# Optimization experiments

Hardware: AMD Instinct MI355X
Metric: run time of the kernel (lower is better)

The kernel has to match this reference:

```python
import jax, jax.numpy as jnp
import numpy as np

NUM_HEADS = 16
LN_EPS = 1e-5


def _layer_norm(x, g, b):
    m = x.mean(-1, keepdims=True)
    v = x.var(-1, keepdims=True)
    return (x - m) / jnp.sqrt(v + LN_EPS) * g + b


def setup_inputs() -> dict:
    key = jax.random.key(0)
    ks = jax.random.split(key, 4)
    Bq, Bk, Nk, C = 128, 128, 256, 1024
    return {
        "qx": jax.random.normal(ks[0], (Bq, 1, C), jnp.float32),
        "kx": jax.random.normal(ks[1], (Bk, Nk, C), jnp.float32),
        "gq": jnp.ones((C,), jnp.float32),
        "bq": jnp.zeros((C,), jnp.float32),
        "gk": jnp.ones((C,), jnp.float32),
        "bk": jnp.zeros((C,), jnp.float32),
        "Wq": jax.random.normal(ks[2], (C, C), jnp.float32) * (C ** -0.5),
        "Wk": jax.random.normal(ks[3], (C, C), jnp.float32) * (C ** -0.5),
    }


def reference(qx, kx, gq, bq, gk, bk, Wq, Wk):
    H = NUM_HEADS
    Bq, _, C = qx.shape  # qx: [Bq, 1, C]
    Bk, Nk, _ = kx.shape  # kx: [Bk, Nk, C]
    hd = C // H
    scale = hd ** -0.5
    # LayerNorm + linear projections (nn.Linear: x @ W.T, no bias)
    q = (_layer_norm(qx, gq, bq) @ Wq.T).reshape(Bq, H, hd)       # [Bq, H, hd] (Nq=1 squeezed)
    k = (_layer_norm(kx, gk, bk) @ Wk.T).reshape(Bk, Nk, H, hd)   # [Bk, Nk, H, hd]
    # Full bipartite cross-batch attention scores: [Bq, Bk, H, Nk]
    attn = jnp.einsum('qhc,knhc->qkhn', q, k) * scale
    attn = jax.nn.softmax(attn, axis=-1)
    # v = kx broadcast over heads in original einsum 'khnc,qkhn->qkc';
    # equivalent: sum attn over heads, then contract over Nk.
    w = attn.sum(axis=2)                                           # [Bq, Bk, Nk]
    x = jnp.einsum('knc,qkn->qkc', kx, w)                          # [Bq, Bk, C]
    return x
```

## Files before the change

kernel.cpp:

```cpp
#include <hip/hip_runtime.h>


typedef unsigned short ushort_t;
typedef __bf16 bf16x8 __attribute__((ext_vector_type(8)));
typedef float f32x4 __attribute__((ext_vector_type(4)));

#define AS1 __attribute__((address_space(1)))
#define AS3 __attribute__((address_space(3)))

__device__ __forceinline__ void gload_lds16(const void* g, void* l) {
  __builtin_amdgcn_global_load_lds((const AS1 unsigned int*)g, (AS3 unsigned int*)l, 16, 0, 0);
}

__device__ __forceinline__ ushort_t f2bf(float f) {
  unsigned u = __float_as_uint(f);
  unsigned r = u + 0x7FFFu + ((u >> 16) & 1u);
  return (ushort_t)(r >> 16);
}

__global__ __launch_bounds__(256) void cvt_bf16_kernel(const float* __restrict__ src,
                                                       ushort_t* __restrict__ dst, int n4) {
  int i = blockIdx.x * 256 + threadIdx.x;
  if (i < n4) {
    float4 v = ((const float4*)src)[i];
    ushort4 o;
    o.x = f2bf(v.x); o.y = f2bf(v.y); o.z = f2bf(v.z); o.w = f2bf(v.w);
    ((ushort4*)dst)[i] = o;
  }
}

__global__ __launch_bounds__(256) void ln_kernel(const float* __restrict__ kx,
                                                 const float* __restrict__ qx,
                                                 const float* __restrict__ gk,
                                                 const float* __restrict__ bk,
                                                 const float* __restrict__ gq,
                                                 const float* __restrict__ bq,
                                                 const float* __restrict__ WqF,
                                                 ushort_t* __restrict__ kln,
                                                 ushort_t* __restrict__ qproj) {
  const int tid = threadIdx.x, lane = tid & 63, wid = tid >> 6;

  if (blockIdx.x < 128) {
    const int ti = blockIdx.x * 4 + wid;
    const int mq = ti >> 6, nq = ti & 63;
    const int g = lane >> 4, rr = lane & 15;

    float s = 0.f, s2 = 0.f;
    {
      const float* p = qx + (size_t)(mq * 16 + (lane & 15)) * 1024 + (lane >> 4) * 256;
      #pragma unroll 8
      for (int i = 0; i < 64; ++i) {
        float4 v = ((const float4*)p)[i];
        s  += v.x + v.y + v.z + v.w;
        s2 += v.x*v.x + v.y*v.y + v.z*v.z + v.w*v.w;
      }
    }
    s  += __shfl_xor(s, 16);  s2 += __shfl_xor(s2, 16);
    s  += __shfl_xor(s, 32);  s2 += __shfl_xor(s2, 32);
    const float mean = s * (1.0f / 1024.0f);
    const float var  = s2 * (1.0f / 1024.0f) - mean * mean;
    const float rstd = rsqrtf(var + 1e-5f);

    const float* qa = qx  + (size_t)(mq * 16 + rr) * 1024;
    const float* wb = WqF + (size_t)(nq * 16 + rr) * 1024;

    f32x4 qacc0 = (f32x4){0.f, 0.f, 0.f, 0.f};
    f32x4 qacc1 = (f32x4){0.f, 0.f, 0.f, 0.f};
    #pragma unroll 4
    for (int kk = 0; kk < 32; kk += 2) {
      #pragma unroll
      for (int e = 0; e < 2; ++e) {
        const int co = (kk + e) * 32 + g * 8;
        float4 a0 = *(const float4*)(qa + co);
        float4 a1 = *(const float4*)(qa + co + 4);
        float4 g0 = *(const float4*)(gq + co);
        float4 g1 = *(const float4*)(gq + co + 4);
        float4 b0 = *(const float4*)(bq + co);
        float4 b1 = *(const float4*)(bq + co + 4);
        float4 w0 = *(const float4*)(wb + co);
        float4 w1 = *(const float4*)(wb + co + 4);
        bf16x8 af, bf;
        af[0] = (__bf16)((a0.x - mean) * rstd * g0.x + b0.x);
        af[1] = (__bf16)((a0.y - mean) * rstd * g0.y + b0.y);
        af[2] = (__bf16)((a0.z - mean) * rstd * g0.z + b0.z);
        af[3] = (__bf16)((a0.w - mean) * rstd * g0.w + b0.w);
        af[4] = (__bf16)((a1.x - mean) * rstd * g1.x + b1.x);
        af[5] = (__bf16)((a1.y - mean) * rstd * g1.y + b1.y);
        af[6] = (__bf16)((a1.z - mean) * rstd * g1.z + b1.z);
        af[7] = (__bf16)((a1.w - mean) * rstd * g1.w + b1.w);
        bf[0] = (__bf16)w0.x; bf[1] = (__bf16)w0.y; bf[2] = (__bf16)w0.z; bf[3] = (__bf16)w0.w;
        bf[4] = (__bf16)w1.x; bf[5] = (__bf16)w1.y; bf[6] = (__bf16)w1.z; bf[7] = (__bf16)w1.w;
        if (e == 0) qacc0 = __builtin_amdgcn_mfma_f32_16x16x32_bf16(af, bf, qacc0, 0, 0, 0);
        else        qacc1 = __builtin_amdgcn_mfma_f32_16x16x32_bf16(af, bf, qacc1, 0, 0, 0);
      }
    }
    #pragma unroll
    for (int rg = 0; rg < 4; ++rg)
      qproj[(size_t)(mq * 16 + (g << 2) + rg) * 1024 + nq * 16 + rr] =
          f2bf(qacc0[rg] + qacc1[rg]);
    return;
  }

  const int row = (blockIdx.x - 128) * 4 + wid;
  const float* src = kx + (size_t)row * 1024;
  ushort_t* dst = kln + (size_t)row * 1024;
  const int c0 = lane * 4;

  float4 v0 = *(const float4*)(src + c0);
  float4 v1 = *(const float4*)(src + c0 + 256);
  float4 v2 = *(const float4*)(src + c0 + 512);
  float4 v3 = *(const float4*)(src + c0 + 768);

  float s  = (v0.x + v0.y + v0.z + v0.w) + (v1.x + v1.y + v1.z + v1.w)
           + (v2.x + v2.y + v2.z + v2.w) + (v3.x + v3.y + v3.z + v3.w);
  float s2 = (v0.x*v0.x + v0.y*v0.y + v0.z*v0.z + v0.w*v0.w)
           + (v1.x*v1.x + v1.y*v1.y + v1.z*v1.z + v1.w*v1.w)
           + (v2.x*v2.x + v2.y*v2.y + v2.z*v2.z + v2.w*v2.w)
           + (v3.x*v3.x + v3.y*v3.y + v3.z*v3.z + v3.w*v3.w);
  #pragma unroll
  for (int off = 1; off < 64; off <<= 1) {
    s  += __shfl_xor(s, off);
    s2 += __shfl_xor(s2, off);
  }
  const float mean = s * (1.0f / 1024.0f);
  const float var  = s2 * (1.0f / 1024.0f) - mean * mean;
  const float rstd = rsqrtf(var + 1e-5f);

  float4 g0 = *(const float4*)(gk + c0);
  float4 g1 = *(const float4*)(gk + c0 + 256);
  float4 g2 = *(const float4*)(gk + c0 + 512);
  float4 g3 = *(const float4*)(gk + c0 + 768);
  float4 b0 = *(const float4*)(bk + c0);
  float4 b1 = *(const float4*)(bk + c0 + 256);
  float4 b2 = *(const float4*)(bk + c0 + 512);
  float4 b3 = *(const float4*)(bk + c0 + 768);

  ushort4 o0, o1, o2, o3;
  o0.x = f2bf((v0.x - mean) * rstd * g0.x + b0.x);
  o0.y = f2bf((v0.y - mean) * rstd * g0.y + b0.y);
  o0.z = f2bf((v0.z - mean) * rstd * g0.z + b0.z);
  o0.w = f2bf((v0.w - mean) * rstd * g0.w + b0.w);
  o1.x = f2bf((v1.x - mean) * rstd * g1.x + b1.x);
  o1.y = f2bf((v1.y - mean) * rstd * g1.y + b1.y);
  o1.z = f2bf((v1.z - mean) * rstd * g1.z + b1.z);
  o1.w = f2bf((v1.w - mean) * rstd * g1.w + b1.w);
  o2.x = f2bf((v2.x - mean) * rstd * g2.x + b2.x);
  o2.y = f2bf((v2.y - mean) * rstd * g2.y + b2.y);
  o2.z = f2bf((v2.z - mean) * rstd * g2.z + b2.z);
  o2.w = f2bf((v2.w - mean) * rstd * g2.w + b2.w);
  o3.x = f2bf((v3.x - mean) * rstd * g3.x + b3.x);
  o3.y = f2bf((v3.y - mean) * rstd * g3.y + b3.y);
  o3.z = f2bf((v3.z - mean) * rstd * g3.z + b3.z);
  o3.w = f2bf((v3.w - mean) * rstd * g3.w + b3.w);

  *(ushort4*)(dst + c0)       = o0;
  *(ushort4*)(dst + c0 + 256) = o1;
  *(ushort4*)(dst + c0 + 512) = o2;
  *(ushort4*)(dst + c0 + 768) = o3;
}

__global__ __launch_bounds__(512, 2) void gemm256_kernel(const ushort_t* __restrict__ A,
                                                         const ushort_t* __restrict__ Bt,
                                                         ushort_t* __restrict__ Cpk,
                                                         int M, int N) {
  __shared__ ushort_t lds[4][2][256 * 32];

  const int tid = threadIdx.x, lane = tid & 63, wid = tid >> 6;
  const int g = lane >> 4, rr = lane & 15;
  const int wr = wid >> 2, wc = wid & 3;

  const int Mt = M >> 8, Nt = N >> 8;
  const int nwg = Mt * Nt;
  const int qq = nwg >> 3, r8 = nwg & 7;
  const int xcd = blockIdx.x & 7, idx = blockIdx.x >> 3;
  const int wg = (xcd < r8 ? xcd * (qq + 1) : r8 * (qq + 1) + (xcd - r8) * qq) + idx;
  const int mt = wg / Nt, nt = wg - mt * Nt;
  const size_t m0 = (size_t)mt << 8, n0 = (size_t)nt << 8;

  const int s_r  = lane >> 2;
  const int s_gr = (lane & 3) ^ (s_r & 3);

  const ushort_t* Abase = A  + m0 * 1024;
  const ushort_t* Bbase = Bt + n0 * 1024;

  f32x4 acc[8][4];
  #pragma unroll
  for (int i = 0; i < 8; ++i)
    #pragma unroll
    for (int j = 0; j < 4; ++j) acc[i][j] = (f32x4){0.f, 0.f, 0.f, 0.f};

  auto stageA = [&](int kt) {
    const int k0 = kt << 5;
    ushort_t* dst = &lds[kt & 3][0][0];
    #pragma unroll
    for (int it = 0; it < 2; ++it) {
      int ci = (wid << 1) | it;
      int r  = (ci << 4) + s_r;
      gload_lds16(Abase + (size_t)r * 1024 + k0 + (s_gr << 3), dst + (ci << 9));
    }
  };
  auto stageB = [&](int kt) {
    const int k0 = kt << 5;
    ushort_t* dst = &lds[kt & 3][1][0];
    #pragma unroll
    for (int it = 0; it < 2; ++it) {
      int ci = (wid << 1) | it;
      int r  = (ci << 4) + s_r;
      gload_lds16(Bbase + (size_t)r * 1024 + k0 + (s_gr << 3), dst + (ci << 9));
    }
  };

  stageA(0); stageB(0); stageA(1); stageB(1); stageA(2); stageB(2);
  asm volatile("s_waitcnt vmcnt(8)" ::: "memory");
  __builtin_amdgcn_s_barrier();

  const int rsw = rr & 3;

  #pragma unroll 1
  for (int u = 0; u < 29; ++u) {
    const ushort_t* as = &lds[u & 3][0][0];
    const ushort_t* bs = &lds[u & 3][1][0];
    bf16x8 af[8];
    {
      #pragma unroll
      for (int i = 0; i < 8; ++i) {
        int r = (wr << 7) + (i << 4) + rr;
        af[i] = *(const bf16x8*)&as[(r << 5) + ((g ^ rsw) << 3)];
      }
      int r0 = (wc << 6) + rr;
      bf16x8 b0 = *(const bf16x8*)&bs[(r0 << 5) + ((g ^ rsw) << 3)];
      int r1 = (wc << 6) + 16 + rr;
      bf16x8 b1 = *(const bf16x8*)&bs[(r1 << 5) + ((g ^ rsw) << 3)];
      stageA(u + 3);
      __builtin_amdgcn_s_setprio(1);
      #pragma unroll
      for (int i = 0; i < 8; ++i) {
        acc[i][0] = __builtin_amdgcn_mfma_f32_16x16x32_bf16(af[i], b0, acc[i][0], 0, 0, 0);
        acc[i][1] = __builtin_amdgcn_mfma_f32_16x16x32_bf16(af[i], b1, acc[i][1], 0, 0, 0);
      }
      __builtin_amdgcn_s_setprio(0);
      __builtin_amdgcn_s_barrier();
    }
    {
      int r2 = (wc << 6) + 32 + rr;
      bf16x8 b2 = *(const bf16x8*)&bs[(r2 << 5) + ((g ^ rsw) << 3)];
      int r3 = (wc << 6) + 48 + rr;
      bf16x8 b3 = *(const bf16x8*)&bs[(r3 << 5) + ((g ^ rsw) << 3)];
      stageB(u + 3);
      __builtin_amdgcn_s_setprio(1);
      #pragma unroll
      for (int i = 0; i < 8; ++i) {
        acc[i][2] = __builtin_amdgcn_mfma_f32_16x16x32_bf16(af[i], b2, acc[i][2], 0, 0, 0);
        acc[i][3] = __builtin_amdgcn_mfma_f32_16x16x32_bf16(af[i], b3, acc[i][3], 0, 0, 0);
      }
      __builtin_amdgcn_s_setprio(0);
      asm volatile("s_waitcnt vmcnt(8)" ::: "memory");
      __builtin_amdgcn_s_barrier();
    }
  }

  asm volatile("s_waitcnt vmcnt(0)" ::: "memory");
  __builtin_amdgcn_s_barrier();
  #pragma unroll 1
  for (int u = 29; u < 32; ++u) {
    const ushort_t* as = &lds[u & 3][0][0];
    const ushort_t* bs = &lds[u & 3][1][0];
    bf16x8 af2[8], bfj[4];
    #pragma unroll
    for (int i = 0; i < 8; ++i) {
      int r = (wr << 7) + (i << 4) + rr;
      af2[i] = *(const bf16x8*)&as[(r << 5) + ((g ^ rsw) << 3)];
    }
    #pragma unroll
    for (int j = 0; j < 4; ++j) {
      int r = (wc << 6) + (j << 4) + rr;
      bfj[j] = *(const bf16x8*)&bs[(r << 5) + ((g ^ rsw) << 3)];
    }
    #pragma unroll
    for (int i = 0; i < 8; ++i)
      #pragma unroll
      for (int j = 0; j < 4; ++j)
        acc[i][j] = __builtin_amdgcn_mfma_f32_16x16x32_bf16(af2[i], bfj[j], acc[i][j], 0, 0, 0);
  }

  #pragma unroll
  for (int i = 0; i < 8; ++i)
    #pragma unroll
    for (int j = 0; j < 4; ++j)
      #pragma unroll
      for (int rg = 0; rg < 4; ++rg) {
        size_t row = m0 + (wr << 7) + (i << 4) + (g << 2) + rg;
        size_t col = n0 + (wc << 6) + (j << 4) + rr;
        int kb = (int)(row >> 8), t = (int)((row >> 4) & 15), r16 = (int)(row & 15);
        int h = (int)(col >> 6), ch = (int)(col & 63);
        size_t odx = ((((size_t)kb * 16 + h) * 16 + t) << 10)
                   + ((ch >> 5) << 9) + (((ch >> 3) & 3) << 7) + (r16 << 3) + (ch & 7);
        Cpk[odx] = f2bf(acc[i][j][rg]);
      }
}

__global__ __launch_bounds__(256, 3) void scores_kernel(const ushort_t* __restrict__ qp,
                                                        const ushort_t* __restrict__ kpk,
                                                        ushort_t* __restrict__ wbuf) {
  __shared__ float pbuf[2][16][258];

  const int tid = threadIdx.x, lane = tid & 63, wid = tid >> 6;
  const int g = lane >> 4, rr = lane & 15;

  const int b = blockIdx.x;
  const int wg = (b & 7) * 128 + (b >> 3);
  const int kb = wg >> 3;
  const int q0 = (wg & 7) << 4;

  const int hs = wid;

  float w_acc[16][4];
  #pragma unroll
  for (int t = 0; t < 16; ++t)
    #pragma unroll
    for (int r = 0; r < 4; ++r) w_acc[t][r] = 0.f;

  const ushort_t* qrow = qp + (size_t)(q0 + rr) * 1024;
  const ushort_t* kbb  = kpk + ((size_t)kb * 16) * 16384 + g * 128 + rr * 8;

  for (int hp = 0; hp < 4; ++hp) {
    const int h = hp * 4 + hs;
    const int co = h * 64 + g * 8;
    bf16x8 aq0 = *(const bf16x8*)(qrow + co);
    bf16x8 aq1 = *(const bf16x8*)(qrow + co + 32);
    const ushort_t* hb = kbb + (size_t)h * 16384;
    f32x4 s[16];
    #pragma unroll
    for (int t = 0; t < 16; ++t) {
      bf16x8 b0 = *(const bf16x8*)(hb + t * 1024);
      bf16x8 b1 = *(const bf16x8*)(hb + t * 1024 + 512);
      f32x4 a = (f32x4){0.f, 0.f, 0.f, 0.f};
      a = __builtin_amdgcn_mfma_f32_16x16x32_bf16(aq0, b0, a, 0, 0, 0);
      a = __builtin_amdgcn_mfma_f32_16x16x32_bf16(aq1, b1, a, 0, 0, 0);
      s[t] = a;
    }
    #pragma unroll
    for (int r = 0; r < 4; ++r) {
      float mx = s[0][r];
      #pragma unroll
      for (int t = 1; t < 16; ++t) mx = fmaxf(mx, s[t][r]);
      mx = fmaxf(mx, __shfl_xor(mx, 1));
      mx = fmaxf(mx, __shfl_xor(mx, 2));
      mx = fmaxf(mx, __shfl_xor(mx, 4));
      mx = fmaxf(mx, __shfl_xor(mx, 8));
      float sum = 0.f;
      float e[16];
      #pragma unroll
      for (int t = 0; t < 16; ++t) {
        e[t] = __expf((s[t][r] - mx) * 0.125f);
        sum += e[t];
      }
      sum += __shfl_xor(sum, 1);
      sum += __shfl_xor(sum, 2);
      sum += __shfl_xor(sum, 4);
      sum += __shfl_xor(sum, 8);
      float inv = 1.0f / sum;
      #pragma unroll
      for (int t = 0; t < 16; ++t) w_acc[t][r] += e[t] * inv;
    }
  }

  __syncthreads();
  if (hs >= 2) {
    #pragma unroll
    for (int t = 0; t < 16; ++t)
      #pragma unroll
      for (int r = 0; r < 4; ++r)
        pbuf[hs - 2][(g << 2) + r][t * 16 + rr] = w_acc[t][r];
  }
  __syncthreads();
  if (hs < 2) {
    #pragma unroll
    for (int t = 0; t < 16; ++t)
      #pragma unroll
      for (int r = 0; r < 4; ++r)
        w_acc[t][r] += pbuf[hs][(g << 2) + r][t * 16 + rr];
    if (hs == 1) {
      #pragma unroll
      for (int t = 0; t < 16; ++t)
        #pragma unroll
        for (int r = 0; r < 4; ++r)
          pbuf[1][(g << 2) + r][t * 16 + rr] = w_acc[t][r];
    }
  }
  __syncthreads();
  if (hs == 0) {
    ushort_t* wb = wbuf + (size_t)kb * 32768;
    #pragma unroll
    for (int t = 0; t < 16; ++t)
      #pragma unroll
      for (int r = 0; r < 4; ++r) {
        float v = w_acc[t][r] + pbuf[1][(g << 2) + r][t * 16 + rr];
        wb[(size_t)(q0 + (g << 2) + r) * 256 + t * 16 + rr] = f2bf(v);
      }
  }
}

__global__ __launch_bounds__(256, 4) void pv_kernel(const ushort_t* __restrict__ wbuf,
                                                    const float* __restrict__ kx,
                                                    float* __restrict__ xout) {
  const int tid = threadIdx.x, lane = tid & 63, wid = tid >> 6;
  const int g = lane >> 4, rr = lane & 15;

  const int b = blockIdx.x;
  const int wg = (b & 7) * 128 + (b >> 3);
  const int kb = wg >> 3;
  const int c0 = (wg & 7) * 128;

  const int wr = wid >> 1, wc = wid & 1;

  f32x4 acc[4][4];
  #pragma unroll
  for (int i = 0; i < 4; ++i)
    #pragma unroll
    for (int j = 0; j < 4; ++j) acc[i][j] = (f32x4){0.f, 0.f, 0.f, 0.f};

  const ushort_t* wb = wbuf + (size_t)kb * 32768;
  const float* kxb = kx + (size_t)kb * 256 * 1024;

  for (int nc = 0; nc < 8; ++nc) {
    const int n0 = nc * 32 + g * 8;
    bf16x8 af[4];
    #pragma unroll
    for (int i = 0; i < 4; ++i) {
      int q = (wr << 6) + (i << 4) + rr;
      af[i] = *(const bf16x8*)(wb + (size_t)q * 256 + n0);
    }
    #pragma unroll
    for (int j = 0; j < 4; ++j) {
      int c = c0 + (wc << 6) + (j << 4) + rr;
      const float* src = kxb + (size_t)n0 * 1024 + c;
      float f[8];
      #pragma unroll
      for (int jj = 0; jj < 8; ++jj) f[jj] = src[(size_t)jj * 1024];
      bf16x8 bb;
      #pragma unroll
      for (int jj = 0; jj < 8; ++jj) bb[jj] = (__bf16)f[jj];
      #pragma unroll
      for (int i = 0; i < 4; ++i)
        acc[i][j] = __builtin_amdgcn_mfma_f32_16x16x32_bf16(af[i], bb, acc[i][j], 0, 0, 0);
    }
  }

  #pragma unroll
  for (int i = 0; i < 4; ++i)
    #pragma unroll
    for (int j = 0; j < 4; ++j)
      #pragma unroll
      for (int rg = 0; rg < 4; ++rg) {
        int q = (wr << 6) + (i << 4) + (g << 2) + rg;
        int c = c0 + (wc << 6) + (j << 4) + rr;
        xout[((size_t)q * 128 + kb) * 1024 + c] = acc[i][j][rg];
      }
}

extern "C" void kernel_launch(void* const* d_in, const int* in_sizes, int n_in,
                              void* d_out, int out_size, void* d_ws, size_t ws_size,
                              hipStream_t stream) {
  const float* qx = (const float*)d_in[0];
  const float* kx = (const float*)d_in[1];
  const float* gq = (const float*)d_in[2];
  const float* bq = (const float*)d_in[3];
  const float* gk = (const float*)d_in[4];
  const float* bk = (const float*)d_in[5];
  const float* Wq = (const float*)d_in[6];
  const float* Wk = (const float*)d_in[7];

  char* ws = (char*)d_ws;
  ushort_t* kkp   = (ushort_t*)(ws);
  ushort_t* qproj = (ushort_t*)(ws + 67108864);
  ushort_t* wbuf  = (ushort_t*)(ws + 67371008);
  ushort_t* Wkb   = (ushort_t*)(ws + 67371008 + 2359296);
  ushort_t* kln  = (ushort_t*)d_out;
  float*    xout = (float*)d_out;

  cvt_bf16_kernel<<<1024, 256, 0, stream>>>(Wk, Wkb, 262144);
  ln_kernel<<<128 + 8192, 256, 0, stream>>>(kx, qx, gk, bk, gq, bq, Wq, kln, qproj);
  gemm256_kernel<<<512, 512, 0, stream>>>(kln, Wkb, kkp, 32768, 1024);
  scores_kernel<<<1024, 256, 0, stream>>>(qproj, kkp, wbuf);
  pv_kernel<<<1024, 256, 0, stream>>>(wbuf, kx, xout);
}
```

Measured before the change: 268.8 us.

## Stage kx tiles through swizzled LDS in pv_kernel and fuse Wk conversion into LN launch

The PV kernel previously read kx from global memory with strided scalar loads, eight rows apart per lane. It now loads 32x128 fp32 tiles with coalesced float4 loads into double-buffered, XOR-swizzled LDS, prefetching the next tile into registers, and builds the MFMA B fragments from LDS. Separately, the Wk fp32-to-bf16 conversion becomes extra blocks of the LN kernel, which removes one launch. The cost is 32KB of LDS per block plus a barrier each iteration, which may lower occupancy under launch_bounds(256,4).

```diff
diff --git a/kernel.cpp b/kernel.cpp
--- a/kernel.cpp
+++ b/kernel.cpp
@@ -16,17 +16,6 @@
   unsigned u = __float_as_uint(f);
   unsigned r = u + 0x7FFFu + ((u >> 16) & 1u);
   return (ushort_t)(r >> 16);
-}
-
-__global__ __launch_bounds__(256) void cvt_bf16_kernel(const float* __restrict__ src,
-                                                       ushort_t* __restrict__ dst, int n4) {
-  int i = blockIdx.x * 256 + threadIdx.x;
-  if (i < n4) {
-    float4 v = ((const float4*)src)[i];
-    ushort4 o;
-    o.x = f2bf(v.x); o.y = f2bf(v.y); o.z = f2bf(v.z); o.w = f2bf(v.w);
-    ((ushort4*)dst)[i] = o;
-  }
 }
 
 __global__ __launch_bounds__(256) void ln_kernel(const float* __restrict__ kx,
@@ -36,9 +25,20 @@
                                                  const float* __restrict__ gq,
                                                  const float* __restrict__ bq,
                                                  const float* __restrict__ WqF,
+                                                 const float* __restrict__ WkF,
+                                                 ushort_t* __restrict__ Wkb,
                                                  ushort_t* __restrict__ kln,
                                                  ushort_t* __restrict__ qproj) {
   const int tid = threadIdx.x, lane = tid & 63, wid = tid >> 6;
+
+  if (blockIdx.x >= 8320) {
+    int i = (blockIdx.x - 8320) * 256 + tid;
+    float4 v = ((const float4*)WkF)[i];
+    ushort4 o;
+    o.x = f2bf(v.x); o.y = f2bf(v.y); o.z = f2bf(v.z); o.w = f2bf(v.w);
+    ((ushort4*)Wkb)[i] = o;
+    return;
+  }
 
   if (blockIdx.x < 128) {
     const int ti = blockIdx.x * 4 + wid;
@@ -404,6 +404,8 @@
 __global__ __launch_bounds__(256, 4) void pv_kernel(const ushort_t* __restrict__ wbuf,
                                                     const float* __restrict__ kx,
                                                     float* __restrict__ xout) {
+  __shared__ float kxs[2][32][128];
+
   const int tid = threadIdx.x, lane = tid & 63, wid = tid >> 6;
   const int g = lane >> 4, rr = lane & 15;
 
@@ -414,6 +416,10 @@
 
   const int wr = wid >> 1, wc = wid & 1;
 
+  const int srow = tid >> 3;
+  const int sgran = tid & 7;
+  const int swz = (srow >> 3) << 2;
+
   f32x4 acc[4][4];
   #pragma unroll
   for (int i = 0; i < 4; ++i)
@@ -421,9 +427,32 @@
     for (int j = 0; j < 4; ++j) acc[i][j] = (f32x4){0.f, 0.f, 0.f, 0.f};
 
   const ushort_t* wb = wbuf + (size_t)kb * 32768;
-  const float* kxb = kx + (size_t)kb * 256 * 1024;
-
+  const float* kxb = kx + ((size_t)kb * 256) * 1024 + c0;
+
+  float4 stg[4];
+  {
+    const float* srcrow = kxb + (size_t)srow * 1024;
+    #pragma unroll
+    for (int l = 0; l < 4; ++l) stg[l] = *(const float4*)(srcrow + ((sgran + l * 8) << 2));
+  }
+
+  #pragma unroll 1
   for (int nc = 0; nc < 8; ++nc) {
+    {
+      float* dstrow = &kxs[nc & 1][srow][0];
+      #pragma unroll
+      for (int l = 0; l < 4; ++l) {
+        int cgp = (sgran + l * 8) ^ swz;
+        *(float4*)(dstrow + (cgp << 2)) = stg[l];
+      }
+    }
+    if (nc < 7) {
+      const float* srcrow = kxb + (size_t)((nc + 1) * 32 + srow) * 1024;
+      #pragma unroll
+      for (int l = 0; l < 4; ++l) stg[l] = *(const float4*)(srcrow + ((sgran + l * 8) << 2));
+    }
+    __syncthreads();
+
     const int n0 = nc * 32 + g * 8;
     bf16x8 af[4];
     #pragma unroll
@@ -431,16 +460,14 @@
       int q = (wr << 6) + (i << 4) + rr;
       af[i] = *(const bf16x8*)(wb + (size_t)q * 256 + n0);
     }
+    const float (*kt)[128] = kxs[nc & 1];
     #pragma unroll
     for (int j = 0; j < 4; ++j) {
-      int c = c0 + (wc << 6) + (j << 4) + rr;
-      const float* src = kxb + (size_t)n0 * 1024 + c;
-      float f[8];
-      #pragma unroll
-      for (int jj = 0; jj < 8; ++jj) f[jj] = src[(size_t)jj * 1024];
+      int cl = (wc << 6) + (j << 4) + rr;
+      int cidx = ((((cl >> 2) ^ (g << 2)) << 2) + (cl & 3));
       bf16x8 bb;
       #pragma unroll
-      for (int jj = 0; jj < 8; ++jj) bb[jj] = (__bf16)f[jj];
+      for (int jj = 0; jj < 8; ++jj) bb[jj] = (__bf16)kt[(g << 3) + jj][cidx];
       #pragma unroll
       for (int i = 0; i < 4; ++i)
         acc[i][j] = __builtin_amdgcn_mfma_f32_16x16x32_bf16(af[i], bb, acc[i][j], 0, 0, 0);
@@ -479,8 +506,8 @@
   ushort_t* kln  = (ushort_t*)d_out;
   float*    xout = (float*)d_out;
 
-  cvt_bf16_kernel<<<1024, 256, 0, stream>>>(Wk, Wkb, 262144);
-  ln_kernel<<<128 + 8192, 256, 0, stream>>>(kx, qx, gk, bk, gq, bq, Wq, kln, qproj);
+  ln_kernel<<<128 + 8192 + 1024, 256, 0, stream>>>(kx, qx, gk, bk, gq, bq, Wq, Wk,
+                                                   Wkb, kln, qproj);
   gemm256_kernel<<<512, 512, 0, stream>>>(kln, Wkb, kkp, 32768, 1024);
   scores_kernel<<<1024, 256, 0, stream>>>(qproj, kkp, wbuf);
   pv_kernel<<<1024, 256, 0, stream>>>(wbuf, kx, xout);
```

Measured after the change: 275.1 us. +2.4%, slower.

## Double K-tile depth in projection GEMM with asymmetric A/B LDS buffering

Applied to the files above, without the earlier changes.

Reworks the bf16 GEMM main loop to stage 64-wide K slices instead of 32-wide ones. A is triple-buffered and B double-buffered in LDS, with a new XOR swizzle. Each K step now uses one wait plus barrier instead of two barriers, and a separate tail loop is no longer needed. This is meant to cut synchronization overhead and raise the number of MFMAs issued per barrier. In exchange, LDS use rises to 160KB and prefetch runs only one to two stages ahead, which may expose global-load latency.

```diff
diff --git a/kernel.cpp b/kernel.cpp
--- a/kernel.cpp
+++ b/kernel.cpp
@@ -163,7 +163,8 @@
                                                          const ushort_t* __restrict__ Bt,
                                                          ushort_t* __restrict__ Cpk,
                                                          int M, int N) {
-  __shared__ ushort_t lds[4][2][256 * 32];
+  __shared__ ushort_t Abuf[3][16384];
+  __shared__ ushort_t Bbuf[2][16384];
 
   const int tid = threadIdx.x, lane = tid & 63, wid = tid >> 6;
   const int g = lane >> 4, rr = lane & 15;
@@ -177,9 +178,6 @@
   const int mt = wg / Nt, nt = wg - mt * Nt;
   const size_t m0 = (size_t)mt << 8, n0 = (size_t)nt << 8;
 
-  const int s_r  = lane >> 2;
-  const int s_gr = (lane & 3) ^ (s_r & 3);
-
   const ushort_t* Abase = A  + m0 * 1024;
   const ushort_t* Bbase = Bt + n0 * 1024;
 
@@ -189,98 +187,87 @@
     #pragma unroll
     for (int j = 0; j < 4; ++j) acc[i][j] = (f32x4){0.f, 0.f, 0.f, 0.f};
 
-  auto stageA = [&](int kt) {
-    const int k0 = kt << 5;
-    ushort_t* dst = &lds[kt & 3][0][0];
-    #pragma unroll
-    for (int it = 0; it < 2; ++it) {
-      int ci = (wid << 1) | it;
-      int r  = (ci << 4) + s_r;
-      gload_lds16(Abase + (size_t)r * 1024 + k0 + (s_gr << 3), dst + (ci << 9));
+  auto stA = [&](int kt) {
+    ushort_t* dst = &Abuf[kt % 3][0];
+    #pragma unroll
+    for (int l = 0; l < 4; ++l) {
+      int ix = l * 512 + tid;
+      int r  = ix >> 3;
+      int gs = (ix & 7) ^ (((r >> 2) & 1) << 1);
+      gload_lds16(Abase + (size_t)r * 1024 + (kt << 6) + (gs << 3), dst + ix * 8);
     }
   };
-  auto stageB = [&](int kt) {
-    const int k0 = kt << 5;
-    ushort_t* dst = &lds[kt & 3][1][0];
-    #pragma unroll
-    for (int it = 0; it < 2; ++it) {
-      int ci = (wid << 1) | it;
-      int r  = (ci << 4) + s_r;
-      gload_lds16(Bbase + (size_t)r * 1024 + k0 + (s_gr << 3), dst + (ci << 9));
+  auto stB = [&](int kt) {
+    ushort_t* dst = &Bbuf[kt & 1][0];
+    #pragma unroll
+    for (int l = 0; l < 4; ++l) {
+      int ix = l * 512 + tid;
+      int r  = ix >> 3;
+      int gs = (ix & 7) ^ (((r >> 2) & 1) << 1);
+      gload_lds16(Bbase + (size_t)r * 1024 + (kt << 6) + (gs << 3), dst + ix * 8);
     }
   };
 
-  stageA(0); stageB(0); stageA(1); stageB(1); stageA(2); stageB(2);
-  asm volatile("s_waitcnt vmcnt(8)" ::: "memory");
+  stA(0); stB(0); stA(1);
+  asm volatile("s_waitcnt vmcnt(4)" ::: "memory");
   __builtin_amdgcn_s_barrier();
 
-  const int rsw = rr & 3;
+  const int sw = ((rr >> 2) & 1) << 1;
 
   #pragma unroll 1
-  for (int u = 0; u < 29; ++u) {
-    const ushort_t* as = &lds[u & 3][0][0];
-    const ushort_t* bs = &lds[u & 3][1][0];
-    bf16x8 af[8];
+  for (int j = 0; j < 16; ++j) {
+    const ushort_t* as = &Abuf[j % 3][0];
+    const ushort_t* bs = &Bbuf[j & 1][0];
+
     {
+      bf16x8 af[8], bf[4];
       #pragma unroll
       for (int i = 0; i < 8; ++i) {
         int r = (wr << 7) + (i << 4) + rr;
-        af[i] = *(const bf16x8*)&as[(r << 5) + ((g ^ rsw) << 3)];
-      }
-      int r0 = (wc << 6) + rr;
-      bf16x8 b0 = *(const bf16x8*)&bs[(r0 << 5) + ((g ^ rsw) << 3)];
-      int r1 = (wc << 6) + 16 + rr;
-      bf16x8 b1 = *(const bf16x8*)&bs[(r1 << 5) + ((g ^ rsw) << 3)];
-      stageA(u + 3);
+        af[i] = *(const bf16x8*)&as[(r << 6) + ((g ^ sw) << 3)];
+      }
+      #pragma unroll
+      for (int jj = 0; jj < 4; ++jj) {
+        int r = (wc << 6) + (jj << 4) + rr;
+        bf[jj] = *(const bf16x8*)&bs[(r << 6) + ((g ^ sw) << 3)];
+      }
+      if (j < 15) stB(j + 1);
+      if (j < 14) stA(j + 2);
       __builtin_amdgcn_s_setprio(1);
       #pragma unroll
+      for (int i = 0; i < 8; ++i)
+        #pragma unroll
+        for (int jj = 0; jj < 4; ++jj)
+          acc[i][jj] = __builtin_amdgcn_mfma_f32_16x16x32_bf16(af[i], bf[jj], acc[i][jj], 0, 0, 0);
+      __builtin_amdgcn_s_setprio(0);
+    }
+    {
+      bf16x8 af[8], bf[4];
+      #pragma unroll
       for (int i = 0; i < 8; ++i) {
-        acc[i][0] = __builtin_amdgcn_mfma_f32_16x16x32_bf16(af[i], b0, acc[i][0], 0, 0, 0);
-        acc[i][1] = __builtin_amdgcn_mfma_f32_16x16x32_bf16(af[i], b1, acc[i][1], 0, 0, 0);
-      }
+        int r = (wr << 7) + (i << 4) + rr;
+        af[i] = *(const bf16x8*)&as[(r << 6) + (((4 + g) ^ sw) << 3)];
+      }
+      #pragma unroll
+      for (int jj = 0; jj < 4; ++jj) {
+        int r = (wc << 6) + (jj << 4) + rr;
+        bf[jj] = *(const bf16x8*)&bs[(r << 6) + (((4 + g) ^ sw) << 3)];
+      }
+      __builtin_amdgcn_s_setprio(1);
+      #pragma unroll
+      for (int i = 0; i < 8; ++i)
+        #pragma unroll
+        for (int jj = 0; jj < 4; ++jj)
+          acc[i][jj] = __builtin_amdgcn_mfma_f32_16x16x32_bf16(af[i], bf[jj], acc[i][jj], 0, 0, 0);
       __builtin_amdgcn_s_setprio(0);
-      __builtin_amdgcn_s_barrier();
-    }
-    {
-      int r2 = (wc << 6) + 32 + rr;
-      bf16x8 b2 = *(const bf16x8*)&bs[(r2 << 5) + ((g ^ rsw) << 3)];
-      int r3 = (wc << 6) + 48 + rr;
-      bf16x8 b3 = *(const bf16x8*)&bs[(r3 << 5) + ((g ^ rsw) << 3)];
-      stageB(u + 3);
-      __builtin_amdgcn_s_setprio(1);
-      #pragma unroll
-      for (int i = 0; i < 8; ++i) {
-        acc[i][2] = __builtin_amdgcn_mfma_f32_16x16x32_bf16(af[i], b2, acc[i][2], 0, 0, 0);
-        acc[i][3] = __builtin_amdgcn_mfma_f32_16x16x32_bf16(af[i], b3, acc[i][3], 0, 0, 0);
-      }
-      __builtin_amdgcn_s_setprio(0);
-      asm volatile("s_waitcnt vmcnt(8)" ::: "memory");
-      __builtin_amdgcn_s_barrier();
-    }
-  }
-
-  asm volatile("s_waitcnt vmcnt(0)" ::: "memory");
-  __builtin_amdgcn_s_barrier();
-  #pragma unroll 1
-  for (int u = 29; u < 32; ++u) {
-    const ushort_t* as = &lds[u & 3][0][0];
-    const ushort_t* bs = &lds[u & 3][1][0];
-    bf16x8 af2[8], bfj[4];
-    #pragma unroll
-    for (int i = 0; i < 8; ++i) {
-      int r = (wr << 7) + (i << 4) + rr;
-      af2[i] = *(const bf16x8*)&as[(r << 5) + ((g ^ rsw) << 3)];
-    }
-    #pragma unroll
-    for (int j = 0; j < 4; ++j) {
-      int r = (wc << 6) + (j << 4) + rr;
-      bfj[j] = *(const bf16x8*)&bs[(r << 5) + ((g ^ rsw) << 3)];
-    }
-    #pragma unroll
-    for (int i = 0; i < 8; ++i)
-      #pragma unroll
-      for (int j = 0; j < 4; ++j)
-        acc[i][j] = __builtin_amdgcn_mfma_f32_16x16x32_bf16(af2[i], bfj[j], acc[i][j], 0, 0, 0);
+      if (j < 14) {
+        asm volatile("s_waitcnt vmcnt(4)" ::: "memory");
+        __builtin_amdgcn_s_barrier();
+      } else if (j == 14) {
+        asm volatile("s_waitcnt vmcnt(0)" ::: "memory");
+        __builtin_amdgcn_s_barrier();
+      }
+    }
   }
 
   #pragma unroll
```

After: 265.7 us. About the same (-1.1%).
